# Optimization experiments

Hardware: AMD Instinct MI355X
Metric: run time of the kernel (lower is better)

The kernel has to match this reference:

```python
import jax, jax.numpy as jnp
import numpy as np

R = 16
N = 524288          # hash table size per level
F = 2               # features per entry
MIN_RES, MAX_RES = 16, 2048
PRIME = 2654435761  # spatial hash prime (as in the torch module)
H = R * F           # MLP width = 32
M = 1048576         # number of query points

# resolutions exactly as in NGP.__init__
RESOLUTIONS = np.round(
    np.logspace(np.log2(MIN_RES), np.log2(MAX_RES), R, base=2)
).astype(np.float32)


def setup_inputs() -> dict:
    key = jax.random.key(0)
    ks = jax.random.split(key, 8)
    coords = jax.random.uniform(ks[0], (M, 2), dtype=jnp.float32)
    hash_features = jax.random.normal(ks[1], (R, N, F), dtype=jnp.float32)
    s = 1.0 / np.sqrt(H)
    W0 = jax.random.uniform(ks[2], (H, H), dtype=jnp.float32, minval=-s, maxval=s)
    b0 = jax.random.uniform(ks[3], (H,), dtype=jnp.float32, minval=-s, maxval=s)
    W1 = jax.random.uniform(ks[4], (H, H), dtype=jnp.float32, minval=-s, maxval=s)
    b1 = jax.random.uniform(ks[5], (H,), dtype=jnp.float32, minval=-s, maxval=s)
    W2 = jax.random.uniform(ks[6], (H, 3), dtype=jnp.float32, minval=-s, maxval=s)
    b2 = jax.random.uniform(ks[7], (3,), dtype=jnp.float32, minval=-s, maxval=s)
    return {"coords": coords, "hash_features": hash_features,
            "W0": W0, "b0": b0, "W1": W1, "b1": b1, "W2": W2, "b2": b2}


def _bilerp_hash(coords, hash_features):
    """coords [M,2] in [0,1); hash_features [R,N,F] -> [M, R*F]."""
    res = jnp.asarray(RESOLUTIONS)  # [R]
    prime = jnp.uint32(PRIME)
    n = jnp.uint32(N)

    def level(res_r, table_r):  # table_r: [N,F]
        x = coords * res_r                    # [M,2]
        xf = jnp.floor(x)
        w = x - xf                            # bilinear weights [M,2]
        xi = xf.astype(jnp.uint32)
        x0, y0 = xi[:, 0], xi[:, 1]

        def look(xx, yy):
            idx = (xx ^ (prime * yy)) % n     # spatial hash
            return table_r[idx]               # gather [M,F]

        wx, wy = w[:, :1], w[:, 1:]
        return (look(x0, y0) * (1 - wx) * (1 - wy)
                + look(x0, y0 + 1) * (1 - wx) * wy
                + look(x0 + 1, y0) * wx * (1 - wy)
                + look(x0 + 1, y0 + 1) * wx * wy)  # [M,F]

    feats = jax.vmap(level)(res, hash_features)   # [R,M,F]
    return jnp.transpose(feats, (1, 0, 2)).reshape(coords.shape[0], -1)  # [M,R*F]


def reference(coords, hash_features, W0, b0, W1, b1, W2, b2):
    f = _bilerp_hash(coords, hash_features)          # [M, 32]
    h = jax.nn.leaky_relu(f @ W0 + b0, 0.01)
    h = jax.nn.leaky_relu(h @ W1 + b1, 0.01)
    return h @ W2 + b2                               # [M, 3]
```

## Files before the change

### kernel.cpp

```cpp
#include <hip/hip_runtime.h>
#include <cmath>

#define R_LEVELS 16
#define N_TAB    524288u
#define N_MASK   (N_TAB - 1u)
#define PRIME_H  2654435761u
#define M_PTS    1048576
#define BDIM     64
#define NBUCK    (BDIM * BDIM)
#define SBLK     256
#define STHR     1024
#define SPB      (M_PTS / SBLK)
#define SITER    (SPB / STHR)
#define XSTRIDE  36
#define NFRAG    384

typedef __attribute__((ext_vector_type(8)))  short bf16x8;
typedef __attribute__((ext_vector_type(16))) float f32x16;

union FragU { bf16x8 v; uint4 q; unsigned u[4]; uint2 u2[2]; unsigned short s[8]; };

struct ResArr { float r[R_LEVELS]; };

__device__ __forceinline__ unsigned pack_hi(float f0, float f1) {
    return __builtin_amdgcn_perm(__float_as_uint(f1), __float_as_uint(f0), 0x07060302u);
}
__device__ __forceinline__ unsigned pack_lo(float f0, float f1) {
    const float l0 = f0 - __uint_as_float(__float_as_uint(f0) & 0xffff0000u);
    const float l1 = f1 - __uint_as_float(__float_as_uint(f1) & 0xffff0000u);
    unsigned r;
    asm("v_cvt_pk_bf16_f32 %0, %1, %2" : "=v"(r) : "v"(l0), "v"(l1));
    return r;
}

__device__ __forceinline__ unsigned bucket_of(float x, float y) {
    unsigned bx = (unsigned)(x * (float)BDIM); if (bx >= BDIM) bx = BDIM - 1;
    unsigned by = (unsigned)(y * (float)BDIM); if (by >= BDIM) by = BDIM - 1;
    unsigned m = 0;
    #pragma unroll
    for (int i = 0; i < 6; ++i)
        m |= (((bx >> i) & 1u) << (2 * i)) | (((by >> i) & 1u) << (2 * i + 1));
    return m;
}

__global__ __launch_bounds__(STHR) void hist_k(const float2* __restrict__ coords,
                                               unsigned short* __restrict__ C) {
    __shared__ unsigned h[NBUCK];
    const int t = threadIdx.x;
    const int w = blockIdx.x;
    #pragma unroll
    for (int i = t; i < NBUCK; i += STHR) h[i] = 0u;
    __syncthreads();
    #pragma unroll
    for (int k = 0; k < SITER; ++k) {
        const int p = w * SPB + k * STHR + t;
        const float2 c = coords[p];
        atomicAdd(&h[bucket_of(c.x, c.y)], 1u);
    }
    __syncthreads();
    #pragma unroll
    for (int i = t; i < NBUCK; i += STHR)
        C[(size_t)w * NBUCK + i] = (unsigned short)h[i];
}

__global__ __launch_bounds__(256) void scanw_k(unsigned short* __restrict__ C,
                                               unsigned* __restrict__ T) {
    const int b = blockIdx.x * 256 + threadIdx.x;
    unsigned s = 0;
    for (int w = 0; w < SBLK; ++w) {
        const size_t i = (size_t)w * NBUCK + b;
        const unsigned v = C[i];
        C[i] = (unsigned short)s;
        s += v;
    }
    T[b] = s;
}

__global__ __launch_bounds__(256) void scan_k(const unsigned* __restrict__ T,
                                              unsigned* __restrict__ B) {
    __shared__ unsigned part[256];
    const int t = threadIdx.x;
    unsigned loc[16];
    unsigned sum = 0;
    #pragma unroll
    for (int k = 0; k < 16; ++k) {
        const unsigned c = T[t * 16 + k];
        loc[k] = sum;
        sum += c;
    }
    part[t] = sum;
    __syncthreads();
    for (int off = 1; off < 256; off <<= 1) {
        const unsigned v = (t >= off) ? part[t - off] : 0u;
        __syncthreads();
        part[t] += v;
        __syncthreads();
    }
    const unsigned base = (t > 0) ? part[t - 1] : 0u;
    #pragma unroll
    for (int k = 0; k < 16; ++k)
        B[t * 16 + k] = base + loc[k];
}

__global__ __launch_bounds__(STHR) void scatter_k(const float2* __restrict__ coords,
                                                  const unsigned short* __restrict__ C,
                                                  const unsigned* __restrict__ B,
                                                  float2* __restrict__ sxy,
                                                  unsigned* __restrict__ sidx) {
    __shared__ unsigned off[NBUCK];
    const int t = threadIdx.x;
    const int w = blockIdx.x;
    #pragma unroll
    for (int i = t; i < NBUCK; i += STHR)
        off[i] = B[i] + (unsigned)C[(size_t)w * NBUCK + i];
    __syncthreads();
    #pragma unroll
    for (int k = 0; k < SITER; ++k) {
        const int p = w * SPB + k * STHR + t;
        const float2 c = coords[p];
        const unsigned b = bucket_of(c.x, c.y);
        const unsigned pos = atomicAdd(&off[b], 1u);
        sxy[pos] = c;
        sidx[pos] = (unsigned)p;
    }
}

__global__ __launch_bounds__(64) void wprep_k(const float* __restrict__ W0,
                                              const float* __restrict__ W1,
                                              const float* __restrict__ W2,
                                              const float* __restrict__ b2,
                                              uint4* __restrict__ wbuf,
                                              float* __restrict__ b2p) {
    const int lane = threadIdx.x;
    const int l31 = lane & 31;
    const int h   = lane >> 5;
    const float* Ws[3] = {W0, W1, W2};
    const int ncols[3] = {32, 32, 3};
    for (int l = 0; l < 3; ++l) {
        for (int kc = 0; kc < 2; ++kc) {
            FragU H, L;
            for (int e = 0; e < 8; ++e) {
                const int k = kc*16 + (e>>2)*8 + h*4 + (e&3);
                const float w = (l31 < ncols[l]) ? Ws[l][k*ncols[l] + l31] : 0.f;
                const unsigned short hi = (unsigned short)(__float_as_uint(w) >> 16);
                const float rem = w - __uint_as_float((unsigned)hi << 16);
                const unsigned u = __float_as_uint(rem);
                const unsigned short lo = (unsigned short)((u + 0x7fffu + ((u >> 16) & 1u)) >> 16);
                H.s[e] = hi;
                L.s[e] = lo;
            }
            const int fi = (l*2 + kc)*64 + lane;
            wbuf[fi]         = H.q;
            wbuf[NFRAG + fi] = L.q;
        }
    }
    if (lane < 32) b2p[lane] = (lane < 3) ? b2[lane] : 0.f;
}

__global__ __launch_bounds__(256, 4) void ngp_mfma(
    const float2* __restrict__ pts,
    const unsigned* __restrict__ sidx,
    const float* __restrict__ hashf,
    const uint4* __restrict__ wbuf,
    const float* __restrict__ b0,
    const float* __restrict__ b1,
    const float* __restrict__ b2p,
    float* __restrict__ out, ResArr res)
{
    __shared__ unsigned short X[256 * XSTRIDE];

    const unsigned nwg = gridDim.x;
    const unsigned chunk = nwg >> 3;
    const unsigned sb = (blockIdx.x & 7u) * chunk + (blockIdx.x >> 3);
    const int tid = threadIdx.x;
    const int p = (int)(sb * 256u) + tid;

    const float2 c = pts[p];

    float f[32];
    #pragma unroll
    for (int ck = 0; ck < 2; ++ck) {
        float2 v00[8], v01[8], v10[8], v11[8];
        float wxs[8], wys[8];
        #pragma unroll
        for (int j = 0; j < 8; ++j) {
            const int r = ck * 8 + j;
            const float rr = res.r[r];
            const float x = c.x * rr;
            const float y = c.y * rr;
            const float xf = floorf(x);
            const float yf = floorf(y);
            wxs[j] = x - xf;
            wys[j] = y - yf;
            const unsigned x0 = (unsigned)xf;
            const unsigned y0 = (unsigned)yf;
            const unsigned hy0 = PRIME_H * y0;
            const unsigned hy1 = PRIME_H * (y0 + 1u);
            const unsigned i00 = (x0 ^ hy0) & N_MASK;
            const unsigned i01 = (x0 ^ hy1) & N_MASK;
            const unsigned i10 = ((x0 + 1u) ^ hy0) & N_MASK;
            const unsigned i11 = ((x0 + 1u) ^ hy1) & N_MASK;
            const float2* tab = (const float2*)hashf + ((size_t)r << 19);
            v00[j] = tab[i00];
            v01[j] = tab[i01];
            v10[j] = tab[i10];
            v11[j] = tab[i11];
        }
        #pragma unroll
        for (int j = 0; j < 8; ++j) {
            const float wx = wxs[j], wy = wys[j];
            const float w00 = (1.f - wx) * (1.f - wy);
            const float w01 = (1.f - wx) * wy;
            const float w10 = wx * (1.f - wy);
            const float w11 = wx * wy;
            const int r = ck * 8 + j;
            f[2*r+0] = v00[j].x*w00 + v01[j].x*w01 + v10[j].x*w10 + v11[j].x*w11;
            f[2*r+1] = v00[j].y*w00 + v01[j].y*w01 + v10[j].y*w10 + v11[j].y*w11;
        }
    }

    const int lane = tid & 63;
    const int wv   = tid >> 6;
    const int l31  = lane & 31;
    const int h    = lane >> 5;
    const int tb0  = wv * 64;
    const int tb1  = wv * 64 + 32;
    const int rowo = tid * XSTRIDE;

    auto ldx = [&](int ptl, int kc) -> FragU {
        FragU r;
        const int off = ptl * XSTRIDE + kc * 16 + h * 4;
        r.u2[0] = *(const uint2*)&X[off];
        r.u2[1] = *(const uint2*)&X[off + 8];
        return r;
    };

    #pragma unroll
    for (int q = 0; q < 8; ++q) {
        uint2 ph;
        ph.x = pack_hi(f[4*q+0], f[4*q+1]);
        ph.y = pack_hi(f[4*q+2], f[4*q+3]);
        *(uint2*)&X[rowo + 4*q] = ph;
    }
    FragU Ah0 = ldx(tb0 + l31, 0);
    FragU Ah1 = ldx(tb0 + l31, 1);
    FragU Bh0 = ldx(tb1 + l31, 0);
    FragU Bh1 = ldx(tb1 + l31, 1);

    #pragma unroll
    for (int q = 0; q < 8; ++q) {
        uint2 pl;
        pl.x = pack_lo(f[4*q+0], f[4*q+1]);
        pl.y = pack_lo(f[4*q+2], f[4*q+3]);
        *(uint2*)&X[rowo + 4*q] = pl;
    }
    FragU Al0 = ldx(tb0 + l31, 0);
    FragU Al1 = ldx(tb0 + l31, 1);
    FragU Bl0 = ldx(tb1 + l31, 0);
    FragU Bl1 = ldx(tb1 + l31, 1);

    auto bias_init = [&](const float* b) -> f32x16 {
        f32x16 a;
        #pragma unroll
        for (int q = 0; q < 4; ++q) {
            const float4 t = *(const float4*)(b + 8*q + 4*h);
            a[4*q+0] = t.x; a[4*q+1] = t.y; a[4*q+2] = t.z; a[4*q+3] = t.w;
        }
        return a;
    };

    f32x16 a0, a1;

    auto layer = [&](int l, const float* b) {
        FragU wh0, wl0, wh1, wl1;
        wh0.q = wbuf[(l*2+0)*64 + lane];
        wl0.q = wbuf[NFRAG + (l*2+0)*64 + lane];
        wh1.q = wbuf[(l*2+1)*64 + lane];
        wl1.q = wbuf[NFRAG + (l*2+1)*64 + lane];
        f32x16 A0 = bias_init(b);
        f32x16 A1 = A0;
        A0 = __builtin_amdgcn_mfma_f32_32x32x16_bf16(wh0.v, Ah0.v, A0, 0, 0, 0);
        A0 = __builtin_amdgcn_mfma_f32_32x32x16_bf16(wh0.v, Al0.v, A0, 0, 0, 0);
        A0 = __builtin_amdgcn_mfma_f32_32x32x16_bf16(wl0.v, Ah0.v, A0, 0, 0, 0);
        A0 = __builtin_amdgcn_mfma_f32_32x32x16_bf16(wh1.v, Ah1.v, A0, 0, 0, 0);
        A0 = __builtin_amdgcn_mfma_f32_32x32x16_bf16(wh1.v, Al1.v, A0, 0, 0, 0);
        A0 = __builtin_amdgcn_mfma_f32_32x32x16_bf16(wl1.v, Ah1.v, A0, 0, 0, 0);
        A1 = __builtin_amdgcn_mfma_f32_32x32x16_bf16(wh0.v, Bh0.v, A1, 0, 0, 0);
        A1 = __builtin_amdgcn_mfma_f32_32x32x16_bf16(wh0.v, Bl0.v, A1, 0, 0, 0);
        A1 = __builtin_amdgcn_mfma_f32_32x32x16_bf16(wl0.v, Bh0.v, A1, 0, 0, 0);
        A1 = __builtin_amdgcn_mfma_f32_32x32x16_bf16(wh1.v, Bh1.v, A1, 0, 0, 0);
        A1 = __builtin_amdgcn_mfma_f32_32x32x16_bf16(wh1.v, Bl1.v, A1, 0, 0, 0);
        A1 = __builtin_amdgcn_mfma_f32_32x32x16_bf16(wl1.v, Bh1.v, A1, 0, 0, 0);
        a0 = A0; a1 = A1;
    };

    auto act_repack = [&](const f32x16& a, FragU& xh0, FragU& xl0, FragU& xh1, FragU& xl1) {
        float v[16];
        #pragma unroll
        for (int r = 0; r < 16; ++r) v[r] = fmaxf(a[r], 0.01f * a[r]);
        #pragma unroll
        for (int w = 0; w < 4; ++w) {
            xh0.u[w] = pack_hi(v[2*w],   v[2*w+1]);
            xl0.u[w] = pack_lo(v[2*w],   v[2*w+1]);
            xh1.u[w] = pack_hi(v[8+2*w], v[8+2*w+1]);
            xl1.u[w] = pack_lo(v[8+2*w], v[8+2*w+1]);
        }
    };

    layer(0, b0);
    act_repack(a0, Ah0, Al0, Ah1, Al1);
    act_repack(a1, Bh0, Bl0, Bh1, Bl1);
    layer(1, b1);
    act_repack(a0, Ah0, Al0, Ah1, Al1);
    act_repack(a1, Bh0, Bl0, Bh1, Bl1);
    layer(2, b2p);

    if (h == 0) {
        const int pl0 = (int)(sb * 256u) + tb0 + l31;
        const int pl1 = (int)(sb * 256u) + tb1 + l31;
        const unsigned o0 = sidx ? sidx[pl0] : (unsigned)pl0;
        const unsigned o1 = sidx ? sidx[pl1] : (unsigned)pl1;
        out[(size_t)o0*3 + 0] = a0[0];
        out[(size_t)o0*3 + 1] = a0[1];
        out[(size_t)o0*3 + 2] = a0[2];
        out[(size_t)o1*3 + 0] = a1[0];
        out[(size_t)o1*3 + 1] = a1[1];
        out[(size_t)o1*3 + 2] = a1[2];
    }
}

extern "C" void kernel_launch(void* const* d_in, const int* in_sizes, int n_in,
                              void* d_out, int out_size, void* d_ws, size_t ws_size,
                              hipStream_t stream) {
    ResArr res;
    for (int i = 0; i < R_LEVELS; ++i)
        res.r[i] = (float)nearbyint(exp2(4.0 + (7.0 / 15.0) * (double)i));
    res.r[0] = 16.f;
    res.r[R_LEVELS - 1] = 2048.f;

    const float2* coords = (const float2*)d_in[0];
    const float* hashf   = (const float*)d_in[1];
    const float* W0      = (const float*)d_in[2];
    const float* b0      = (const float*)d_in[3];
    const float* W1      = (const float*)d_in[4];
    const float* b1      = (const float*)d_in[5];
    const float* W2      = (const float*)d_in[6];
    const float* b2      = (const float*)d_in[7];
    float* out           = (float*)d_out;

    const size_t off_C    = 0;
    const size_t off_T    = off_C + (size_t)SBLK * NBUCK * 2;
    const size_t off_B    = off_T + NBUCK * 4;
    const size_t off_sxy  = off_B + NBUCK * 4;
    const size_t off_sidx = off_sxy + (size_t)M_PTS * sizeof(float2);
    const size_t off_wbuf = off_sidx + (size_t)M_PTS * 4;
    const size_t off_b2p  = off_wbuf + 2 * NFRAG * sizeof(uint4);
    const size_t need     = off_b2p + 32 * sizeof(float);
    const size_t need_min = 2 * NFRAG * sizeof(uint4) + 32 * sizeof(float);

    dim3 blockM(256);
    dim3 gridM(M_PTS / 256);

    if (ws_size >= need) {
        unsigned short* C = (unsigned short*)((char*)d_ws + off_C);
        unsigned* T    = (unsigned*)((char*)d_ws + off_T);
        unsigned* B    = (unsigned*)((char*)d_ws + off_B);
        float2*   sxy  = (float2*)((char*)d_ws + off_sxy);
        unsigned* sidx = (unsigned*)((char*)d_ws + off_sidx);
        uint4*    wbuf = (uint4*)((char*)d_ws + off_wbuf);
        float*    b2p  = (float*)((char*)d_ws + off_b2p);

        hipLaunchKernelGGL(wprep_k,   dim3(1), dim3(64), 0, stream, W0, W1, W2, b2, wbuf, b2p);
        hipLaunchKernelGGL(hist_k,    dim3(SBLK), dim3(STHR), 0, stream, coords, C);
        hipLaunchKernelGGL(scanw_k,   dim3(NBUCK / 256), dim3(256), 0, stream, C, T);
        hipLaunchKernelGGL(scan_k,    dim3(1), dim3(256), 0, stream, T, B);
        hipLaunchKernelGGL(scatter_k, dim3(SBLK), dim3(STHR), 0, stream, coords, C, B, sxy, sidx);
        hipLaunchKernelGGL(ngp_mfma,  gridM, blockM, 0, stream,
                           sxy, sidx, hashf, wbuf, b0, b1, b2p, out, res);
    } else if (ws_size >= need_min) {
        uint4* wbuf = (uint4*)d_ws;
        float* b2p  = (float*)((char*)d_ws + 2 * NFRAG * sizeof(uint4));
        hipLaunchKernelGGL(wprep_k,   dim3(1), dim3(64), 0, stream, W0, W1, W2, b2, wbuf, b2p);
        hipLaunchKernelGGL(ngp_mfma,  gridM, blockM, 0, stream,
                           coords, (const unsigned*)nullptr, hashf, wbuf, b0, b1, b2p, out, res);
    }
}
```

Baseline: 123.5 us.

## Refine spatial sort buckets, split column scan into segments, double-buffer hash gathers

Doubles the sort grid to 128x128 Morton buckets, so points handled together lie closer in space and gathers at the fine levels hit the cache more often. The per-bucket scan across 256 blocks is split into eight segments plus a second pass, which raises parallelism in the scan stage. The grid encoding loop is restructured into four chunks of four levels with two register buffers, so one chunk's gathers are in flight while the previous chunk is interpolated. The cost is more workspace, larger 64 KB shared histograms that may lower occupancy in the hist and scatter kernels, one extra launch, and possibly higher register pressure.

```diff
diff --git a/kernel.cpp b/kernel.cpp
--- a/kernel.cpp
+++ b/kernel.cpp
@@ -6,12 +6,14 @@
 #define N_MASK   (N_TAB - 1u)
 #define PRIME_H  2654435761u
 #define M_PTS    1048576
-#define BDIM     64
+#define BDIM     128
 #define NBUCK    (BDIM * BDIM)
 #define SBLK     256
 #define STHR     1024
 #define SPB      (M_PTS / SBLK)
 #define SITER    (SPB / STHR)
+#define NSEG     8
+#define WSEG     (SBLK / NSEG)
 #define XSTRIDE  36
 #define NFRAG    384
 
@@ -38,7 +40,7 @@
     unsigned by = (unsigned)(y * (float)BDIM); if (by >= BDIM) by = BDIM - 1;
     unsigned m = 0;
     #pragma unroll
-    for (int i = 0; i < 6; ++i)
+    for (int i = 0; i < 7; ++i)
         m |= (((bx >> i) & 1u) << (2 * i)) | (((by >> i) & 1u) << (2 * i + 1));
     return m;
 }
@@ -63,16 +65,34 @@
         C[(size_t)w * NBUCK + i] = (unsigned short)h[i];
 }
 
-__global__ __launch_bounds__(256) void scanw_k(unsigned short* __restrict__ C,
-                                               unsigned* __restrict__ T) {
-    const int b = blockIdx.x * 256 + threadIdx.x;
+__global__ __launch_bounds__(256) void scanw1_k(unsigned short* __restrict__ C,
+                                                unsigned* __restrict__ P) {
+    const int g = blockIdx.x * 256 + threadIdx.x;
+    const int seg = g >> 14;
+    const int b   = g & (NBUCK - 1);
     unsigned s = 0;
-    for (int w = 0; w < SBLK; ++w) {
+    #pragma unroll
+    for (int k = 0; k < WSEG; ++k) {
+        const int w = seg * WSEG + k;
         const size_t i = (size_t)w * NBUCK + b;
         const unsigned v = C[i];
         C[i] = (unsigned short)s;
         s += v;
     }
+    P[(size_t)seg * NBUCK + b] = s;
+}
+
+__global__ __launch_bounds__(256) void scanw2_k(unsigned* __restrict__ P,
+                                                unsigned* __restrict__ T) {
+    const int b = blockIdx.x * 256 + threadIdx.x;
+    unsigned s = 0;
+    #pragma unroll
+    for (int seg = 0; seg < NSEG; ++seg) {
+        const size_t i = (size_t)seg * NBUCK + b;
+        const unsigned v = P[i];
+        P[i] = s;
+        s += v;
+    }
     T[b] = s;
 }
 
@@ -80,14 +100,8 @@
                                               unsigned* __restrict__ B) {
     __shared__ unsigned part[256];
     const int t = threadIdx.x;
-    unsigned loc[16];
     unsigned sum = 0;
-    #pragma unroll
-    for (int k = 0; k < 16; ++k) {
-        const unsigned c = T[t * 16 + k];
-        loc[k] = sum;
-        sum += c;
-    }
+    for (int k = 0; k < 64; ++k) sum += T[t * 64 + k];
     part[t] = sum;
     __syncthreads();
     for (int off = 1; off < 256; off <<= 1) {
@@ -96,23 +110,26 @@
         part[t] += v;
         __syncthreads();
     }
-    const unsigned base = (t > 0) ? part[t - 1] : 0u;
-    #pragma unroll
-    for (int k = 0; k < 16; ++k)
-        B[t * 16 + k] = base + loc[k];
+    unsigned run = (t > 0) ? part[t - 1] : 0u;
+    for (int k = 0; k < 64; ++k) {
+        B[t * 64 + k] = run;
+        run += T[t * 64 + k];
+    }
 }
 
 __global__ __launch_bounds__(STHR) void scatter_k(const float2* __restrict__ coords,
                                                   const unsigned short* __restrict__ C,
+                                                  const unsigned* __restrict__ P,
                                                   const unsigned* __restrict__ B,
                                                   float2* __restrict__ sxy,
                                                   unsigned* __restrict__ sidx) {
     __shared__ unsigned off[NBUCK];
     const int t = threadIdx.x;
     const int w = blockIdx.x;
+    const int seg = w / WSEG;
     #pragma unroll
     for (int i = t; i < NBUCK; i += STHR)
-        off[i] = B[i] + (unsigned)C[(size_t)w * NBUCK + i];
+        off[i] = B[i] + P[(size_t)seg * NBUCK + i] + (unsigned)C[(size_t)w * NBUCK + i];
     __syncthreads();
     #pragma unroll
     for (int k = 0; k < SITER; ++k) {
@@ -178,46 +195,53 @@
     const float2 c = pts[p];
 
     float f[32];
-    #pragma unroll
-    for (int ck = 0; ck < 2; ++ck) {
-        float2 v00[8], v01[8], v10[8], v11[8];
-        float wxs[8], wys[8];
+    float2 vA[16], vB[16];
+    float2 wA[4], wB[4];
+
+    auto issue = [&](int ck, float2* vv, float2* ww) {
         #pragma unroll
-        for (int j = 0; j < 8; ++j) {
-            const int r = ck * 8 + j;
+        for (int j = 0; j < 4; ++j) {
+            const int r = ck * 4 + j;
             const float rr = res.r[r];
             const float x = c.x * rr;
             const float y = c.y * rr;
             const float xf = floorf(x);
             const float yf = floorf(y);
-            wxs[j] = x - xf;
-            wys[j] = y - yf;
+            ww[j].x = x - xf;
+            ww[j].y = y - yf;
             const unsigned x0 = (unsigned)xf;
             const unsigned y0 = (unsigned)yf;
             const unsigned hy0 = PRIME_H * y0;
             const unsigned hy1 = PRIME_H * (y0 + 1u);
-            const unsigned i00 = (x0 ^ hy0) & N_MASK;
-            const unsigned i01 = (x0 ^ hy1) & N_MASK;
-            const unsigned i10 = ((x0 + 1u) ^ hy0) & N_MASK;
-            const unsigned i11 = ((x0 + 1u) ^ hy1) & N_MASK;
             const float2* tab = (const float2*)hashf + ((size_t)r << 19);
-            v00[j] = tab[i00];
-            v01[j] = tab[i01];
-            v10[j] = tab[i10];
-            v11[j] = tab[i11];
+            vv[4*j+0] = tab[(x0 ^ hy0) & N_MASK];
+            vv[4*j+1] = tab[(x0 ^ hy1) & N_MASK];
+            vv[4*j+2] = tab[((x0 + 1u) ^ hy0) & N_MASK];
+            vv[4*j+3] = tab[((x0 + 1u) ^ hy1) & N_MASK];
         }
+    };
+    auto consume = [&](int ck, const float2* vv, const float2* ww) {
         #pragma unroll
-        for (int j = 0; j < 8; ++j) {
-            const float wx = wxs[j], wy = wys[j];
+        for (int j = 0; j < 4; ++j) {
+            const int r = ck * 4 + j;
+            const float wx = ww[j].x, wy = ww[j].y;
             const float w00 = (1.f - wx) * (1.f - wy);
             const float w01 = (1.f - wx) * wy;
             const float w10 = wx * (1.f - wy);
             const float w11 = wx * wy;
-            const int r = ck * 8 + j;
-            f[2*r+0] = v00[j].x*w00 + v01[j].x*w01 + v10[j].x*w10 + v11[j].x*w11;
-            f[2*r+1] = v00[j].y*w00 + v01[j].y*w01 + v10[j].y*w10 + v11[j].y*w11;
+            f[2*r+0] = vv[4*j+0].x*w00 + vv[4*j+1].x*w01 + vv[4*j+2].x*w10 + vv[4*j+3].x*w11;
+            f[2*r+1] = vv[4*j+0].y*w00 + vv[4*j+1].y*w01 + vv[4*j+2].y*w10 + vv[4*j+3].y*w11;
         }
-    }
+    };
+
+    issue(0, vA, wA);
+    issue(1, vB, wB);
+    consume(0, vA, wA);
+    issue(2, vA, wA);
+    consume(1, vB, wB);
+    issue(3, vB, wB);
+    consume(2, vA, wA);
+    consume(3, vB, wB);
 
     const int lane = tid & 63;
     const int wv   = tid >> 6;
@@ -349,7 +373,8 @@
     float* out           = (float*)d_out;
 
     const size_t off_C    = 0;
-    const size_t off_T    = off_C + (size_t)SBLK * NBUCK * 2;
+    const size_t off_P    = off_C + (size_t)SBLK * NBUCK * 2;
+    const size_t off_T    = off_P + (size_t)NSEG * NBUCK * 4;
     const size_t off_B    = off_T + NBUCK * 4;
     const size_t off_sxy  = off_B + NBUCK * 4;
     const size_t off_sidx = off_sxy + (size_t)M_PTS * sizeof(float2);
@@ -363,6 +388,7 @@
 
     if (ws_size >= need) {
         unsigned short* C = (unsigned short*)((char*)d_ws + off_C);
+        unsigned* P    = (unsigned*)((char*)d_ws + off_P);
         unsigned* T    = (unsigned*)((char*)d_ws + off_T);
         unsigned* B    = (unsigned*)((char*)d_ws + off_B);
         float2*   sxy  = (float2*)((char*)d_ws + off_sxy);
@@ -372,9 +398,10 @@
 
         hipLaunchKernelGGL(wprep_k,   dim3(1), dim3(64), 0, stream, W0, W1, W2, b2, wbuf, b2p);
         hipLaunchKernelGGL(hist_k,    dim3(SBLK), dim3(STHR), 0, stream, coords, C);
-        hipLaunchKernelGGL(scanw_k,   dim3(NBUCK / 256), dim3(256), 0, stream, C, T);
+        hipLaunchKernelGGL(scanw1_k,  dim3(NSEG * NBUCK / 256), dim3(256), 0, stream, C, P);
+        hipLaunchKernelGGL(scanw2_k,  dim3(NBUCK / 256), dim3(256), 0, stream, P, T);
         hipLaunchKernelGGL(scan_k,    dim3(1), dim3(256), 0, stream, T, B);
-        hipLaunchKernelGGL(scatter_k, dim3(SBLK), dim3(STHR), 0, stream, coords, C, B, sxy, sidx);
+        hipLaunchKernelGGL(scatter_k, dim3(SBLK), dim3(STHR), 0, stream, coords, C, P, B, sxy, sidx);
         hipLaunchKernelGGL(ngp_mfma,  gridM, blockM, 0, stream,
                            sxy, sidx, hashf, wbuf, b0, b1, b2p, out, res);
     } else if (ws_size >= need_min) {
```

Result: no change. 123.2 us (-0.2%).
